# Performance work log

Hardware: AMD Instinct MI355X
Metric: run time of the kernel (lower is better)

Reference implementation:

```python
import jax, jax.numpy as jnp
import numpy as np

N, E, C, EMB, NB, L = 20000, 640000, 64, 32, 8, 2
MAX_RADIUS = 2.5
NUM_NEIGHBORS = 32.0
RH = 32  # radial MLP hidden


def setup_inputs() -> dict:
    key = jax.random.key(0)
    ks = jax.random.split(key, 24)
    g = lambda k, shape, fan: (jax.random.normal(k, shape, dtype=jnp.float32) / np.sqrt(fan).astype(np.float32))
    inp = {
        'x': jax.random.normal(ks[0], (N, 6), dtype=jnp.float32),
        'batch': jnp.zeros((N,), dtype=jnp.int64),
        'node_attr': jax.random.randint(ks[1], (N,), 0, 100),
        'edge_src': jax.random.randint(ks[2], (E,), 0, N),
        'edge_dst': jax.random.randint(ks[3], (E,), 0, N),
        'emb_table': jax.random.normal(ks[4], (100, EMB), dtype=jnp.float32),
        'uplift_M': jax.random.normal(ks[5], (C, 2), dtype=jnp.float32),
        'h': jnp.ones((L,), jnp.float32) * 0.01,
        'mix': jnp.ones((L,), jnp.float32) * 0.5,
        'rad_W1': g(ks[6], (L, NB, RH), NB),
        'rad_b1': jnp.zeros((L, RH), jnp.float32),
        'rad_W2': g(ks[7], (L, RH, 2 * C), RH),
        'lin1_s': g(ks[8], (L, C, C), C),
        'lin1_v': g(ks[9], (L, C, C), C),
        'lin2_s': g(ks[10], (L, C, 2 * C), C),
        'lin2_v': g(ks[11], (L, C, C), C),
        'sc_s_w': g(ks[12], (L, C, EMB, 2 * C), C * EMB),
        'sc_v_w': g(ks[13], (L, C, EMB, C), C * EMB),
        'si_s': g(ks[14], (L, C, C), C),
        'si_v': g(ks[15], (L, C, C), C),
    }
    return inp


def _forward(x, batch, node_attr, edge_src, edge_dst, emb_table, uplift_M, h, mix,
             rad_W1, rad_b1, rad_W2, lin1_s, lin1_v, lin2_s, lin2_v,
             sc_s_w, sc_v_w, si_s, si_v):
    n = x.shape[0]
    emb = emb_table[node_attr]                       # [N, EMB] node embedding
    # semi-unitarize uplift matrix: Q = M (M^T M)^{-1/2} == U V^T
    U, _, Vt = jnp.linalg.svd(uplift_M, full_matrices=False)
    Q = U @ Vt                                       # [C, 2]
    xv = x.reshape(n, 2, 3)
    y_s = jnp.zeros((n, C), x.dtype)                 # hidden scalars start at 0
    y_v = jnp.einsum('nkx,ck->ncx', xv, Q)           # uplift vectors [N,C,3]
    y = (y_s, y_v)
    y_old = y
    nbas = jnp.arange(1, NB + 1, dtype=x.dtype)
    inv_nn = 1.0 / np.sqrt(NUM_NEIGHBORS).astype(np.float32)
    for i in range(L):
        pos = x[:, :3]
        ev = pos[edge_src] - pos[edge_dst]           # [E,3]
        elen = jnp.linalg.norm(ev, axis=1)
        safe = jnp.maximum(elen, 1e-9)
        sh = np.float32(np.sqrt(3.0)) * ev / safe[:, None]   # 1x1o SH, component norm
        # bessel radial basis, scaled by sqrt(NB)
        ef = (np.float32(np.sqrt(2.0 / MAX_RADIUS)) *
              jnp.sin(nbas[None, :] * jnp.pi * safe[:, None] / MAX_RADIUS) / safe[:, None])
        ef = ef * np.float32(np.sqrt(NB))
        # smooth cutoff (e3nn tetris style)
        u = 2.0 * (elen / MAX_RADIUS - 1.0)
        cut = jnp.where(u > 0, 0.0, jnp.where(u < -2, 1.0, 0.5 * (1.0 - jnp.cos(jnp.pi * u))))
        ea = cut[:, None] * sh                       # [E,3] edge attr
        # linear pre-mix
        s1 = y[0] @ lin1_s[i]                        # [N,C]
        v1 = jnp.einsum('ncx,cd->ndx', y[1], lin1_v[i])  # [N,C,3]
        # radial MLP -> per-edge TP weights
        w = jax.nn.silu(ef @ rad_W1[i] + rad_b1[i]) @ rad_W2[i]  # [E,2C]
        w1, w2 = w[:, :C], w[:, C:]
        # tensor-product messages: 0e x 1o -> 1o ; 1o . 1o -> 0e
        msg_v = (w1 * s1[edge_src])[:, :, None] * ea[:, None, :]        # [E,C,3]
        msg_s = w2 * jnp.einsum('ecx,ex->ec', v1[edge_src], ea)         # [E,C]
        agg_s = jax.ops.segment_sum(msg_s, edge_dst, num_segments=n) * inv_nn
        agg_v = jax.ops.segment_sum(msg_v, edge_dst, num_segments=n) * inv_nn
        # post linear + node-attr self connection
        out_s = agg_s @ lin2_s[i] + jnp.einsum('nc,ne,ceo->no', y[0], emb, sc_s_w[i])   # [N,2C]
        out_v = (jnp.einsum('ncx,cd->ndx', agg_v, lin2_v[i]) +
                 jnp.einsum('ncx,ne,ceo->nox', y[1], emb, sc_v_w[i]))                   # [N,C,3]
        # gated nonlinearity
        g_s = jax.nn.silu(out_s[:, :C])
        g_v = jax.nn.sigmoid(out_s[:, C:])[:, :, None] * out_v
        # self interaction
        y2_s = y[0] @ si_s[i]
        y2_v = jnp.einsum('ncx,cd->ndx', y[1], si_v[i])
        # leapfrog update
        hh = h[i] * h[i]
        m = mix[i]
        new_s = 2.0 * y[0] - y_old[0] + hh * (m * g_s + (m - 1.0) * y2_s)
        new_v = 2.0 * y[1] - y_old[1] + hh * (m * g_v + (m - 1.0) * y2_v)
        y_old = y
        y = (new_s, new_v)
        x = jnp.einsum('ncx,ck->nkx', new_v, Q).reshape(n, 6)   # project
    return x


def reference(x, batch, node_attr, edge_src, edge_dst, emb_table, uplift_M, h, mix,
              rad_W1, rad_b1, rad_W2, lin1_s, lin1_v, lin2_s, lin2_v,
              sc_s_w, sc_v_w, si_s, si_v):
    return _forward(x, batch, node_attr, edge_src, edge_dst, emb_table, uplift_M, h, mix,
                    rad_W1, rad_b1, rad_W2, lin1_s, lin1_v, lin2_s, lin2_v,
                    sc_s_w, sc_v_w, si_s, si_v)
```

## Files before the change

### kernel.cpp

```cpp
#include <hip/hip_runtime.h>
#include <cstdio>
#include <cstdint>

#define CCH 64
#define EMBD 32
#define NBD 8
#define RHD 32
#define NATTR 100
#define TBINS 64

static constexpr float MAXR    = 2.5f;
static constexpr float INVNN   = 0.17677669529663687f;
static constexpr float EFK     = 2.5298221281347035f;
static constexpr float SQRT3   = 1.7320508075688772f;
static constexpr float PI_F    = 3.14159265358979323846f;

typedef __fp16 v2h __attribute__((ext_vector_type(2)));

__device__ __forceinline__ float sigm_(float x) { return 1.f / (1.f + __expf(-x)); }
__device__ __forceinline__ float silu_(float x) { return x / (1.f + __expf(-x)); }
__device__ __forceinline__ unsigned f2bfu(float f) {
    unsigned u = __float_as_uint(f);
    return (u + 0x7FFF + ((u >> 16) & 1)) >> 16;
}
__device__ __forceinline__ unsigned pack2(float lo, float hi) {
    return f2bfu(lo) | (f2bfu(hi) << 16);
}
__device__ __forceinline__ float ulo(unsigned u) { return __uint_as_float(u << 16); }
__device__ __forceinline__ float uhi(unsigned u) { return __uint_as_float(u & 0xFFFF0000u); }
__device__ __forceinline__ v2h u2h(unsigned u) { v2h h; __builtin_memcpy(&h, &u, 4); return h; }
__device__ __forceinline__ unsigned pkh(float a, float b) {
    v2h h = __builtin_amdgcn_cvt_pkrtz(a, b);
    unsigned u; __builtin_memcpy(&u, &h, 4); return u;
}
__device__ __forceinline__ unsigned short h1(float f) {
    __fp16 h = (__fp16)f; unsigned short s; __builtin_memcpy(&s, &h, 2); return s;
}
__device__ __forceinline__ float dot2(unsigned a, unsigned b, float c) {
    return __builtin_amdgcn_fdot2(u2h(a), u2h(b), c, false);
}
__device__ __forceinline__ float hlo(unsigned u) { v2h h = u2h(u); return (float)h.x; }
__device__ __forceinline__ float hhi(unsigned u) { v2h h = u2h(u); return (float)h.y; }

__global__ void kQ(const float* M, float* Q) {
    int c = threadIdx.x;
    float m0 = M[2*c], m1 = M[2*c+1];
    float a = m0*m0, b = m0*m1, d = m1*m1;
    for (int o = 32; o > 0; o >>= 1) {
        a += __shfl_xor(a, o); b += __shfl_xor(b, o); d += __shfl_xor(d, o);
    }
    float det = a*d - b*b;
    float s = sqrtf(det);
    float t = sqrtf(a + d + 2.f*s);
    float inv = 1.f / (s*t);
    float i00 = (d + s)*inv, i01 = -b*inv, i11 = (a + s)*inv;
    Q[2*c]   = m0*i00 + m1*i01;
    Q[2*c+1] = m0*i01 + m1*i11;
}

__global__ void kRadTab(const float* __restrict__ rW1, const float* __restrict__ rb1,
                        const float* __restrict__ rW2, unsigned* __restrict__ tab) {
    int bin = blockIdx.x;
    int l   = blockIdx.y;
    int lane = threadIdx.x;
    float r = bin * (MAXR / TBINS);
    float safe = fmaxf(r, 1e-9f);
    float invSafe = 1.f / safe;
    float th = PI_F * r * (1.f / MAXR);
    float s0, c0;
    __sincosf(th, &s0, &c0);
    __shared__ float hidS[RHD];
    if (lane < RHD) {
        float hs = rb1[l*RHD + lane];
        float sPrev = 0.f, sCur = s0, twoC = 2.f*c0;
        #pragma unroll
        for (int b = 0; b < NBD; ++b) {
            float efb = EFK * sCur * invSafe;
            hs = fmaf(efb, rW1[(l*NBD + b)*RHD + lane], hs);
            float sN = fmaf(twoC, sCur, -sPrev);
            sPrev = sCur; sCur = sN;
        }
        hidS[lane] = silu_(hs);
    }
    __syncthreads();
    float w1 = 0.f, w2 = 0.f;
    #pragma unroll
    for (int rr = 0; rr < RHD; ++rr) {
        float h = hidS[rr];
        w1 = fmaf(h, rW2[(l*RHD + rr)*128 + lane], w1);
        w2 = fmaf(h, rW2[(l*RHD + rr)*128 + 64 + lane], w2);
    }
    float cut = s0*s0;
    float coef = SQRT3 * cut * invSafe * INVNN;
    tab[((size_t)l*(TBINS+1) + bin)*64 + lane] = pack2(w1*coef, w2*coef);
}

__global__ void kPackW(const float* __restrict__ siv, unsigned* __restrict__ siVp) {
    int l = blockIdx.y;
    int i = blockIdx.x*256 + threadIdx.x;
    int cp = i >> 6, o = i & 63;
    siVp[l*2048 + i] = pkh(siv[l*4096 + (2*cp)*64 + o], siv[l*4096 + (2*cp+1)*64 + o]);
}

__global__ __launch_bounds__(256) void kInitLin(const float* __restrict__ x, const float* __restrict__ Qg,
        const float* __restrict__ L1v,
        float* __restrict__ yAv, float4* __restrict__ pos4,
        uint2* __restrict__ mv, int n) {
    __shared__ unsigned wPk[32*64];
    __shared__ __align__(16) unsigned bc[4][32][4];
    int t = threadIdx.x;
    for (int i = t; i < 32*64; i += 256) {
        int cp = i >> 6, o = i & 63;
        wPk[i] = pkh(L1v[(2*cp)*64 + o], L1v[(2*cp+1)*64 + o]);
    }
    __syncthreads();
    int lane = t & 63;
    int wid = t >> 6;
    float q0 = Qg[2*lane], q1 = Qg[2*lane+1];
    for (int node = blockIdx.x*4 + wid; node < n; node += gridDim.x*4) {
        const float* xr = x + (size_t)node*6;
        float x0 = xr[0], x1 = xr[1], x2 = xr[2], x3 = xr[3], x4 = xr[4], x5 = xr[5];
        float y0 = q0*x0 + q1*x3;
        float y1 = q0*x1 + q1*x4;
        float y2 = q0*x2 + q1*x5;
        float* yv = yAv + (size_t)node*192 + lane*3;
        yv[0] = y0; yv[1] = y1; yv[2] = y2;
        if (lane == 0) pos4[node] = (float4){x0, x1, x2, 0.f};
        {
            unsigned short* p = (unsigned short*)bc[wid][lane >> 1];
            int sub = lane & 1;
            p[0*2+sub] = h1(y0); p[1*2+sub] = h1(y1); p[2*2+sub] = h1(y2);
        }
        float a0 = 0.f, a1 = 0.f, a2 = 0.f;
        #pragma unroll 8
        for (int cp = 0; cp < 32; ++cp) {
            uint4 b = *(const uint4*)&bc[wid][cp][0];
            unsigned wp = wPk[cp*64 + lane];
            a0 = dot2(b.x, wp, a0);
            a1 = dot2(b.y, wp, a1);
            a2 = dot2(b.z, wp, a2);
        }
        mv[(size_t)node*64 + lane] = (uint2){ pack2(a0, a1), pack2(a2, 0.f) };
    }
}

__global__ void kHist(const int* dst, int* cnt, int e) {
    int i = blockIdx.x*blockDim.x + threadIdx.x;
    if (i < e) atomicAdd(&cnt[dst[i]], 1);
}

__global__ void kScan(const int* cnt, int* offs, int* curG0, int* curG1, int n) {
    __shared__ int part[1024];
    int t = threadIdx.x;
    int chunk = (n + 1023) >> 10;
    int lo = t*chunk, hi = min(lo + chunk, n);
    int s = 0;
    for (int i = lo; i < hi; ++i) s += cnt[i];
    part[t] = s;
    __syncthreads();
    for (int o = 1; o < 1024; o <<= 1) {
        int w = (t >= o) ? part[t - o] : 0;
        __syncthreads();
        part[t] += w;
        __syncthreads();
    }
    int run = part[t] - s;
    for (int i = lo; i < hi; ++i) {
        int cv = cnt[i];
        offs[i] = run; curG0[i] = run; curG1[i] = run;
        run += cv;
    }
    if (t == 1023) offs[n] = part[1023];
}

__global__ __launch_bounds__(256) void kGeom(const float4* __restrict__ pos4,
        const int* __restrict__ esrc, const int* __restrict__ edst,
        int* __restrict__ cur, uint4* __restrict__ rec, int e) {
    int i = blockIdx.x*256 + threadIdx.x;
    if (i >= e) return;
    int s = esrc[i], d = edst[i];
    float4 pa = pos4[s], pb = pos4[d];
    float ex = pa.x - pb.x, ey = pa.y - pb.y, ez = pa.z - pb.z;
    float el2 = ex*ex + ey*ey + ez*ez;
    if (el2 >= MAXR*MAXR) return;
    float elen = sqrtf(el2);
    float u = fminf(elen * ((float)TBINS / MAXR), 63.98f);
    int p = atomicAdd(&cur[d], 1);
    rec[p] = (uint4){ (unsigned)s, pkh(ex, ey), pkh(ez, u), 0u };
}

__global__ __launch_bounds__(256) void kT3(const float* __restrict__ embT,
        const float* __restrict__ scs, const float* __restrict__ scv,
        unsigned* __restrict__ TallU) {
    int cp = blockIdx.x, l = blockIdx.y, ag = blockIdx.z;
    int c0 = 2*cp, c1 = c0 + 1;
    __shared__ float sS0[32*128], sS1[32*128], sV0[32*64], sV1[32*64], sE[20*EMBD];
    int t = threadIdx.x;
    const float* p0 = scs + ((size_t)(l*CCH + c0)*EMBD)*128;
    const float* p1 = scs + ((size_t)(l*CCH + c1)*EMBD)*128;
    for (int i = t; i < 32*128; i += 256) { sS0[i] = p0[i]; sS1[i] = p1[i]; }
    const float* q0 = scv + ((size_t)(l*CCH + c0)*EMBD)*64;
    const float* q1 = scv + ((size_t)(l*CCH + c1)*EMBD)*64;
    for (int i = t; i < 32*64; i += 256) { sV0[i] = q0[i]; sV1[i] = q1[i]; }
    const float* eb = embT + (size_t)ag*20*EMBD;
    for (int i = t; i < 20*EMBD; i += 256) sE[i] = eb[i];
    __syncthreads();
    if (t < 128) {
        int o = t;
        for (int a = 0; a < 20; ++a) {
            float acc0 = 0.f, acc1 = 0.f;
            #pragma unroll
            for (int e = 0; e < EMBD; ++e) {
                float ev = sE[a*EMBD + e];
                acc0 = fmaf(ev, sS0[e*128 + o], acc0);
                acc1 = fmaf(ev, sS1[e*128 + o], acc1);
            }
            int aa = ag*20 + a;
            size_t idx = ((size_t)(l*NATTR + aa)*32 + cp)*64 + (o & 63);
            TallU[idx*4 + (o >> 6)] = pkh(acc0, acc1);
        }
    } else if (t < 192) {
        int o = t - 128;
        for (int a = 0; a < 20; ++a) {
            float acc0 = 0.f, acc1 = 0.f;
            #pragma unroll
            for (int e = 0; e < EMBD; ++e) {
                float ev = sE[a*EMBD + e];
                acc0 = fmaf(ev, sV0[e*64 + o], acc0);
                acc1 = fmaf(ev, sV1[e*64 + o], acc1);
            }
            int aa = ag*20 + a;
            size_t idx = ((size_t)(l*NATTR + aa)*32 + cp)*64 + o;
            TallU[idx*4 + 2] = pkh(acc0, acc1);
        }
    }
}

__global__ __launch_bounds__(256) void kLin1(const float* __restrict__ ys, const float* __restrict__ yv,
        const float* __restrict__ L1s, const float* __restrict__ L1v,
        uint2* __restrict__ mv, int n) {
    __shared__ uint2 wPk[32*64];
    __shared__ __align__(16) unsigned bc[4][32][4];
    int t = threadIdx.x;
    for (int i = t; i < 32*64; i += 256) {
        int cp = i >> 6, o = i & 63;
        wPk[i] = (uint2){ pkh(L1s[(2*cp)*64 + o], L1s[(2*cp+1)*64 + o]),
                          pkh(L1v[(2*cp)*64 + o], L1v[(2*cp+1)*64 + o]) };
    }
    __syncthreads();
    int lane = t & 63;
    int wid = t >> 6;
    for (int node = blockIdx.x*4 + wid; node < n; node += gridDim.x*4) {
        float ys_r = ys[(size_t)node*64 + lane];
        const float* yvp = yv + (size_t)node*192 + lane*3;
        float y0 = yvp[0], y1 = yvp[1], y2 = yvp[2];
        {
            unsigned short* p = (unsigned short*)bc[wid][lane >> 1];
            int sub = lane & 1;
            p[0*2+sub] = h1(y0); p[1*2+sub] = h1(y1);
            p[2*2+sub] = h1(y2); p[3*2+sub] = h1(ys_r);
        }
        float as = 0.f, a0 = 0.f, a1 = 0.f, a2 = 0.f;
        #pragma unroll 8
        for (int cp = 0; cp < 32; ++cp) {
            uint4 b = *(const uint4*)&bc[wid][cp][0];
            uint2 wp = wPk[cp*64 + lane];
            as = dot2(b.w, wp.x, as);
            a0 = dot2(b.x, wp.y, a0);
            a1 = dot2(b.y, wp.y, a1);
            a2 = dot2(b.z, wp.y, a2);
        }
        mv[(size_t)node*64 + lane] = (uint2){ pack2(a0, a1), pack2(a2, as) };
    }
}

template<int WITHV>
__global__ __launch_bounds__(256) void kAgg(const uint4* __restrict__ rec,
        const uint2* __restrict__ mv,
        const int* __restrict__ offs, const int* __restrict__ endA,
        const unsigned* __restrict__ tabG,
        float* __restrict__ aggS, float* __restrict__ aggV, int n) {
    __shared__ unsigned tab[(TBINS+1)*64];
    __shared__ float red[4][64][4];
    int t = threadIdx.x;
    for (int i = t; i < (TBINS+1)*64; i += 256) tab[i] = tabG[i];
    __syncthreads();
    int lane = t & 63;
    int wid = t >> 6;

    for (int node = blockIdx.x; node < n; node += gridDim.x) {
        int beg = offs[node], end = endA[node];
        float accS = 0.f, av0 = 0.f, av1 = 0.f, av2 = 0.f;
        int idx = beg + wid;
        uint4 r0 = (uint4){0u,0u,0u,0u}, r1 = r0;
        uint2 m0 = (uint2){0u,0u}, m1 = m0;
        if (idx < end)     { r0 = rec[idx];   m0 = mv[(size_t)r0.x*64 + lane]; }
        if (idx + 4 < end) { r1 = rec[idx+4]; m1 = mv[(size_t)r1.x*64 + lane]; }
        for (; idx < end; idx += 4) {
            uint4 r2 = (uint4){0u,0u,0u,0u};
            uint2 m2 = (uint2){0u,0u};
            if (idx + 8 < end) { r2 = rec[idx+8]; m2 = mv[(size_t)r2.x*64 + lane]; }
            float ex = hlo(r0.y), ey = hhi(r0.y);
            float ez = hlo(r0.z), u = hhi(r0.z);
            int i0 = (int)u;
            float fr = u - (float)i0;
            unsigned t0 = tab[i0*64 + lane];
            unsigned t1 = tab[i0*64 + 64 + lane];
            float w1 = fmaf(fr, ulo(t1) - ulo(t0), ulo(t0));
            float w2 = fmaf(fr, uhi(t1) - uhi(t0), uhi(t0));
            float dv = ulo(m0.x)*ex + uhi(m0.x)*ey + ulo(m0.y)*ez;
            accS = fmaf(w2, dv, accS);
            if (WITHV) {
                float tt = w1 * uhi(m0.y);
                av0 = fmaf(tt, ex, av0); av1 = fmaf(tt, ey, av1); av2 = fmaf(tt, ez, av2);
            }
            r0 = r1; m0 = m1; r1 = r2; m1 = m2;
        }
        red[wid][lane][0] = accS; red[wid][lane][1] = av0;
        red[wid][lane][2] = av1;  red[wid][lane][3] = av2;
        __syncthreads();
        if (wid == 0) {
            float rs = red[0][lane][0] + red[1][lane][0] + red[2][lane][0] + red[3][lane][0];
            aggS[(size_t)node*64 + lane] = rs;
            float r0s = red[0][lane][1] + red[1][lane][1] + red[2][lane][1] + red[3][lane][1];
            float r1s = red[0][lane][2] + red[1][lane][2] + red[2][lane][2] + red[3][lane][2];
            float r2s = red[0][lane][3] + red[1][lane][3] + red[2][lane][3] + red[3][lane][3];
            float* ap = aggV + (size_t)node*192 + lane*3;
            ap[0] = r0s; ap[1] = r1s; ap[2] = r2s;
        }
        __syncthreads();
    }
}

template<int L0>
__global__ __launch_bounds__(256) void kOutComb(const float* __restrict__ ys, const float* __restrict__ yv,
        const float* __restrict__ yoldv,
        const float* __restrict__ aggS, const float* __restrict__ aggV, const int* __restrict__ attr,
        const float* __restrict__ L2s, const float* __restrict__ L2v,
        const uint4* __restrict__ Tall,
        const float* __restrict__ siS, const unsigned* __restrict__ siVp, const float* __restrict__ Qg,
        const float* __restrict__ hArr, const float* __restrict__ mArr, int li,
        float* __restrict__ newS, float* __restrict__ newV,
        float4* __restrict__ pos4out, float* __restrict__ xout6, int n) {
    __shared__ uint4 wAll[32*64];
    __shared__ __align__(16) unsigned bc[4][32][8];
    int t = threadIdx.x;
    for (int i = t; i < 32*64; i += 256) {
        int cp = i >> 6, o = i & 63;
        wAll[i] = (uint4){ pkh(L2s[(2*cp)*128 + o],      L2s[(2*cp+1)*128 + o]),
                           pkh(L2s[(2*cp)*128 + 64 + o], L2s[(2*cp+1)*128 + 64 + o]),
                           pkh(L2v[(2*cp)*64 + o], L2v[(2*cp+1)*64 + o]),
                           L0 ? 0u : pkh(siS[(2*cp)*64 + o], siS[(2*cp+1)*64 + o]) };
    }
    __syncthreads();
    int lane = t & 63;
    int wid = t >> 6;
    unsigned svr[32];
    #pragma unroll
    for (int cp = 0; cp < 32; ++cp) svr[cp] = siVp[cp*64 + lane];
    float hh = hArr[li]; hh *= hh;
    float m = mArr[li];
    float q0 = Qg[2*lane], q1 = Qg[2*lane+1];
    for (int node = blockIdx.x*4 + wid; node < n; node += gridDim.x*4) {
        int a = attr[node];
        const unsigned* tA = (const unsigned*)(Tall + (size_t)a*2048);
        float as_r = aggS[(size_t)node*64 + lane];
        float ys_r = L0 ? 0.f : ys[(size_t)node*64 + lane];
        const float* avp = aggV + (size_t)node*192 + lane*3;
        float av0 = avp[0], av1 = avp[1], av2 = avp[2];
        const float* yvp = yv + (size_t)node*192 + lane*3;
        float by0 = yvp[0], by1 = yvp[1], by2 = yvp[2];
        {
            unsigned short* p = (unsigned short*)bc[wid][lane >> 1];
            int sub = lane & 1;
            p[0*2+sub] = h1(as_r); p[1*2+sub] = L0 ? (unsigned short)0 : h1(ys_r);
            p[2*2+sub] = h1(av0);  p[3*2+sub] = h1(by0);
            p[4*2+sub] = h1(av1);  p[5*2+sub] = h1(by1);
            p[6*2+sub] = h1(av2);  p[7*2+sub] = h1(by2);
        }
        float oS0=0.f, oS1=0.f, ov0=0.f, ov1=0.f, ov2=0.f;
        float q2s=0.f, qv0=0.f, qv1=0.f, qv2=0.f;
        #pragma unroll 4
        for (int cp = 0; cp < 32; ++cp) {
            uint4 bA = *(const uint4*)&bc[wid][cp][0];
            uint4 bB = *(const uint4*)&bc[wid][cp][4];
            uint4 wv4 = wAll[cp*64 + lane];
            if (L0) {
                unsigned tv = tA[(cp*64 + lane)*4 + 2];
                oS0 = dot2(bA.x, wv4.x, oS0);
                oS1 = dot2(bA.x, wv4.y, oS1);
                ov0 = dot2(bA.z, wv4.z, dot2(bA.w, tv, ov0));
                ov1 = dot2(bB.x, wv4.z, dot2(bB.y, tv, ov1));
                ov2 = dot2(bB.z, wv4.z, dot2(bB.w, tv, ov2));
            } else {
                uint4 tw = ((const uint4*)tA)[cp*64 + lane];
                oS0 = dot2(bA.x, wv4.x, dot2(bA.y, tw.x, oS0));
                oS1 = dot2(bA.x, wv4.y, dot2(bA.y, tw.y, oS1));
                ov0 = dot2(bA.z, wv4.z, dot2(bA.w, tw.z, ov0));
                ov1 = dot2(bB.x, wv4.z, dot2(bB.y, tw.z, ov1));
                ov2 = dot2(bB.z, wv4.z, dot2(bB.w, tw.z, ov2));
                q2s = dot2(bA.y, wv4.w, q2s);
            }
            qv0 = dot2(bA.w, svr[cp], qv0);
            qv1 = dot2(bB.y, svr[cp], qv1);
            qv2 = dot2(bB.w, svr[cp], qv2);
        }
        float gs = silu_(oS0);
        float sg = sigm_(oS1);
        float gv0 = sg*ov0, gv1 = sg*ov1, gv2 = sg*ov2;
        float ns, nv0, nv1, nv2;
        if (L0) {
            ns  = hh*m*gs;
            nv0 = by0 + hh*(m*gv0 + (m-1.f)*qv0);
            nv1 = by1 + hh*(m*gv1 + (m-1.f)*qv1);
            nv2 = by2 + hh*(m*gv2 + (m-1.f)*qv2);
        } else {
            const float* yop = yoldv + (size_t)node*192 + lane*3;
            ns  = 2.f*ys_r + hh*(m*gs + (m-1.f)*q2s);
            nv0 = 2.f*by0 - yop[0] + hh*(m*gv0 + (m-1.f)*qv0);
            nv1 = 2.f*by1 - yop[1] + hh*(m*gv1 + (m-1.f)*qv1);
            nv2 = 2.f*by2 - yop[2] + hh*(m*gv2 + (m-1.f)*qv2);
        }
        if (L0) {
            newS[(size_t)node*64 + lane] = ns;
            float* np = newV + (size_t)node*192 + lane*3;
            np[0] = nv0; np[1] = nv1; np[2] = nv2;
        }
        float p00 = nv0*q0, p01 = nv1*q0, p02 = nv2*q0;
        float p10 = nv0*q1, p11 = nv1*q1, p12 = nv2*q1;
        for (int o = 32; o > 0; o >>= 1) {
            p00 += __shfl_xor(p00, o); p01 += __shfl_xor(p01, o); p02 += __shfl_xor(p02, o);
            p10 += __shfl_xor(p10, o); p11 += __shfl_xor(p11, o); p12 += __shfl_xor(p12, o);
        }
        if (lane == 0) {
            if (L0) {
                pos4out[node] = (float4){p00, p01, p02, 0.f};
            } else {
                float* xp = xout6 + (size_t)node*6;
                xp[0] = p00; xp[1] = p01; xp[2] = p02;
                xp[3] = p10; xp[4] = p11; xp[5] = p12;
            }
        }
    }
}

extern "C" void kernel_launch(void* const* d_in, const int* in_sizes, int n_in,
                              void* d_out, int out_size, void* d_ws, size_t ws_size,
                              hipStream_t stream) {
    const float* x        = (const float*)d_in[0];
    const int*   nattr    = (const int*)  d_in[2];
    const int*   esrc     = (const int*)  d_in[3];
    const int*   edst     = (const int*)  d_in[4];
    const float* embT     = (const float*)d_in[5];
    const float* upM      = (const float*)d_in[6];
    const float* hArr     = (const float*)d_in[7];
    const float* mArr     = (const float*)d_in[8];
    const float* rW1      = (const float*)d_in[9];
    const float* rb1      = (const float*)d_in[10];
    const float* rW2      = (const float*)d_in[11];
    const float* l1s      = (const float*)d_in[12];
    const float* l1v      = (const float*)d_in[13];
    const float* l2s      = (const float*)d_in[14];
    const float* l2v      = (const float*)d_in[15];
    const float* scs      = (const float*)d_in[16];
    const float* scv      = (const float*)d_in[17];
    const float* sis      = (const float*)d_in[18];
    const float* siv      = (const float*)d_in[19];
    int n = in_sizes[0] / 6;
    int e = in_sizes[3];
    float* out = (float*)d_out;

    float* w = (float*)d_ws;
    float* Q    = w; w += 128;
    float* yAv  = w; w += (size_t)n*192;
    float* yBs  = w; w += (size_t)n*64;
    float* yBv  = w; w += (size_t)n*192;
    float* aggS = w; w += (size_t)n*64;
    float* aggV = w; w += (size_t)n*192;
    float4* pos4 = (float4*)w; w += (size_t)n*4;
    uint2* mv    = (uint2*)w;  w += (size_t)n*128;
    uint4* Tall  = (uint4*)w;  w += (size_t)2*NATTR*2048*4;
    unsigned* radTab = (unsigned*)w; w += (size_t)2*(TBINS+1)*64;
    unsigned* siVp = (unsigned*)w; w += (size_t)2*2048;
    uint4* rec = (uint4*)w; w += (size_t)e*4;
    int* cnt   = (int*)w;
    int* offs  = cnt + n;
    int* curG0 = offs + (n + 1);
    int* curG1 = curG0 + n;
    size_t need = (size_t)((char*)(curG1 + n) - (char*)d_ws);
    if (need > ws_size) {
        fprintf(stderr, "kernel_launch: ws too small (%zu > %zu)\n", need, ws_size);
        return;
    }

    const int AGG_GRID  = 1792;
    const int OC_GRID   = 1024;
    const int LIN_GRID  = 2048;
    int eb = (e + 255)/256;

    kQ<<<1, 64, 0, stream>>>(upM, Q);
    hipMemsetAsync(cnt, 0, (size_t)n*sizeof(int), stream);
    kHist<<<eb, 256, 0, stream>>>(edst, cnt, e);
    kScan<<<1, 1024, 0, stream>>>(cnt, offs, curG0, curG1, n);
    kT3<<<dim3(32, 2, 5), 256, 0, stream>>>(embT, scs, scv, (unsigned*)Tall);
    kRadTab<<<dim3(TBINS+1, 2), 64, 0, stream>>>(rW1, rb1, rW2, radTab);
    kPackW<<<dim3(8, 2), 256, 0, stream>>>(siv, siVp);
    kInitLin<<<LIN_GRID, 256, 0, stream>>>(x, Q, l1v, yAv, pos4, mv, n);

    kGeom<<<eb, 256, 0, stream>>>(pos4, esrc, edst, curG0, rec, e);
    kAgg<0><<<AGG_GRID, 256, 0, stream>>>(rec, mv, offs, curG0, radTab, aggS, aggV, n);
    kOutComb<1><<<OC_GRID, 256, 0, stream>>>(nullptr, yAv, nullptr, aggS, aggV, nattr,
                                  l2s, l2v, Tall, sis, siVp, Q, hArr, mArr, 0,
                                  yBs, yBv, pos4, out, n);
    kLin1<<<LIN_GRID, 256, 0, stream>>>(yBs, yBv, l1s + 4096, l1v + 4096, mv, n);
    kGeom<<<eb, 256, 0, stream>>>(pos4, esrc, edst, curG1, rec, e);
    kAgg<1><<<AGG_GRID, 256, 0, stream>>>(rec, mv, offs, curG1,
                                  radTab + (size_t)(TBINS+1)*64, aggS, aggV, n);
    kOutComb<0><<<OC_GRID, 256, 0, stream>>>(yBs, yBv, yAv, aggS, aggV, nattr,
                                  l2s + (size_t)64*128, l2v + (size_t)64*64,
                                  Tall + (size_t)NATTR*2048,
                                  sis + 4096, siVp + 2048, Q, hArr, mArr, 1,
                                  nullptr, nullptr, nullptr, out, n);
}
```

Before: 493.3 us.

## Sort nodes by attribute so kOutComb waves reuse per-attribute weight tables

Adds a counting sort of nodes by node_attr (histogram, scan and scatter kernels) and makes each wave of kOutComb process a contiguous chunk of the sorted order instead of a grid-stride loop. Consecutive nodes in a wave then share the same 32 KB per-attribute table Tall[a], so those loads should hit cache more often. The cost is three extra small kernel launches, one atomic scatter, and node reads and writes that are no longer coalesced in node order.

```diff
diff --git a/kernel.cpp b/kernel.cpp
--- a/kernel.cpp
+++ b/kernel.cpp
@@ -171,6 +171,33 @@
         run += cv;
     }
     if (t == 1023) offs[n] = part[1023];
+}
+
+__global__ void kHistA(const int* __restrict__ attr, int* __restrict__ acnt, int n) {
+    int i = blockIdx.x*256 + threadIdx.x;
+    if (i < n) atomicAdd(&acnt[attr[i]], 1);
+}
+__global__ void kScanA(const int* __restrict__ acnt, int* __restrict__ acur) {
+    __shared__ int part[128];
+    int t = threadIdx.x;
+    int v = (t < NATTR) ? acnt[t] : 0;
+    part[t] = v;
+    __syncthreads();
+    for (int o = 1; o < 128; o <<= 1) {
+        int w = (t >= o) ? part[t - o] : 0;
+        __syncthreads();
+        part[t] += w;
+        __syncthreads();
+    }
+    if (t < NATTR) acur[t] = part[t] - v;
+}
+__global__ void kScatterA(const int* __restrict__ attr, int* __restrict__ acur,
+                          int* __restrict__ nodeOrd, int n) {
+    int i = blockIdx.x*256 + threadIdx.x;
+    if (i < n) {
+        int p = atomicAdd(&acur[attr[i]], 1);
+        nodeOrd[p] = i;
+    }
 }
 
 __global__ __launch_bounds__(256) void kGeom(const float4* __restrict__ pos4,
@@ -335,7 +362,8 @@
 template<int L0>
 __global__ __launch_bounds__(256) void kOutComb(const float* __restrict__ ys, const float* __restrict__ yv,
         const float* __restrict__ yoldv,
-        const float* __restrict__ aggS, const float* __restrict__ aggV, const int* __restrict__ attr,
+        const float* __restrict__ aggS, const float* __restrict__ aggV,
+        const int* __restrict__ attr, const int* __restrict__ nodeOrd,
         const float* __restrict__ L2s, const float* __restrict__ L2v,
         const uint4* __restrict__ Tall,
         const float* __restrict__ siS, const unsigned* __restrict__ siVp, const float* __restrict__ Qg,
@@ -361,7 +389,12 @@
     float hh = hArr[li]; hh *= hh;
     float m = mArr[li];
     float q0 = Qg[2*lane], q1 = Qg[2*lane+1];
-    for (int node = blockIdx.x*4 + wid; node < n; node += gridDim.x*4) {
+    int nw = gridDim.x*4;
+    int chunk = (n + nw - 1) / nw;
+    int start = (blockIdx.x*4 + wid) * chunk;
+    int stop = min(start + chunk, n);
+    for (int ii = start; ii < stop; ++ii) {
+        int node = nodeOrd[ii];
         int a = attr[node];
         const unsigned* tA = (const unsigned*)(Tall + (size_t)a*2048);
         float as_r = aggS[(size_t)node*64 + lane];
@@ -487,7 +520,10 @@
     int* offs  = cnt + n;
     int* curG0 = offs + (n + 1);
     int* curG1 = curG0 + n;
-    size_t need = (size_t)((char*)(curG1 + n) - (char*)d_ws);
+    int* acnt  = curG1 + n;
+    int* acur  = acnt + NATTR;
+    int* nodeOrd = acur + NATTR;
+    size_t need = (size_t)((char*)(nodeOrd + n) - (char*)d_ws);
     if (need > ws_size) {
         fprintf(stderr, "kernel_launch: ws too small (%zu > %zu)\n", need, ws_size);
         return;
@@ -497,11 +533,16 @@
     const int OC_GRID   = 1024;
     const int LIN_GRID  = 2048;
     int eb = (e + 255)/256;
+    int nb = (n + 255)/256;
 
     kQ<<<1, 64, 0, stream>>>(upM, Q);
     hipMemsetAsync(cnt, 0, (size_t)n*sizeof(int), stream);
+    hipMemsetAsync(acnt, 0, (size_t)NATTR*sizeof(int), stream);
     kHist<<<eb, 256, 0, stream>>>(edst, cnt, e);
     kScan<<<1, 1024, 0, stream>>>(cnt, offs, curG0, curG1, n);
+    kHistA<<<nb, 256, 0, stream>>>(nattr, acnt, n);
+    kScanA<<<1, 128, 0, stream>>>(acnt, acur);
+    kScatterA<<<nb, 256, 0, stream>>>(nattr, acur, nodeOrd, n);
     kT3<<<dim3(32, 2, 5), 256, 0, stream>>>(embT, scs, scv, (unsigned*)Tall);
     kRadTab<<<dim3(TBINS+1, 2), 64, 0, stream>>>(rW1, rb1, rW2, radTab);
     kPackW<<<dim3(8, 2), 256, 0, stream>>>(siv, siVp);
@@ -509,14 +550,14 @@
 
     kGeom<<<eb, 256, 0, stream>>>(pos4, esrc, edst, curG0, rec, e);
     kAgg<0><<<AGG_GRID, 256, 0, stream>>>(rec, mv, offs, curG0, radTab, aggS, aggV, n);
-    kOutComb<1><<<OC_GRID, 256, 0, stream>>>(nullptr, yAv, nullptr, aggS, aggV, nattr,
+    kOutComb<1><<<OC_GRID, 256, 0, stream>>>(nullptr, yAv, nullptr, aggS, aggV, nattr, nodeOrd,
                                   l2s, l2v, Tall, sis, siVp, Q, hArr, mArr, 0,
                                   yBs, yBv, pos4, out, n);
     kLin1<<<LIN_GRID, 256, 0, stream>>>(yBs, yBv, l1s + 4096, l1v + 4096, mv, n);
     kGeom<<<eb, 256, 0, stream>>>(pos4, esrc, edst, curG1, rec, e);
     kAgg<1><<<AGG_GRID, 256, 0, stream>>>(rec, mv, offs, curG1,
                                   radTab + (size_t)(TBINS+1)*64, aggS, aggV, n);
-    kOutComb<0><<<OC_GRID, 256, 0, stream>>>(yBs, yBv, yAv, aggS, aggV, nattr,
+    kOutComb<0><<<OC_GRID, 256, 0, stream>>>(yBs, yBv, yAv, aggS, aggV, nattr, nodeOrd,
                                   l2s + (size_t)64*128, l2v + (size_t)64*64,
                                   Tall + (size_t)NATTR*2048,
                                   sis + 4096, siVp + 2048, Q, hArr, mArr, 1,
```

Result: slower. 571.5 us (+15.8%).
